# Kernel tuning notes

Hardware: AMD Instinct MI355X
Metric: run time of the kernel (lower is better)

## Reference

```python
import jax, jax.numpy as jnp
import numpy as np

W_SIM, W_REC, W_FREQ, W_IMP, W_TYPE = 0.45, 0.2, 0.15, 0.1, 0.1
TYPE_WEIGHT = 0.9
DECAY_HALF_LIFE = 200.0
TEMPERATURE = 0.07
LN_EPS = 1e-5


def _l2norm(v, axis=-1):
    # matches torch F.normalize (eps=1e-12 clamp on the norm)
    n = jnp.linalg.norm(v, axis=axis, keepdims=True)
    return v / jnp.maximum(n, 1e-12)


def setup_inputs() -> dict:
    key = jax.random.key(0)
    ks = jax.random.split(key, 8)
    B, D, S = 16384, 2048, 64
    s = 1.0 / np.sqrt(D)
    x = jax.random.normal(ks[0], (B, D), jnp.float32)
    prototypes = _l2norm(jax.random.normal(ks[1], (S, D), jnp.float32))
    proto_conf = jax.random.uniform(ks[2], (S,), jnp.float32)
    proto_age = jax.random.uniform(ks[3], (S,), jnp.float32)
    proto_evidence = jnp.ones((S,), jnp.float32)
    W_in = jax.random.normal(ks[4], (D, D), jnp.float32) * s
    b_in = jnp.zeros((D,), jnp.float32)
    Wr1 = jax.random.normal(ks[5], (D // 2, D), jnp.float32) * s
    br1 = jnp.zeros((D // 2,), jnp.float32)
    Wr2 = jax.random.normal(ks[6], (4, D // 2), jnp.float32) * (1.0 / np.sqrt(D // 2))
    br2 = jnp.zeros((4,), jnp.float32)
    W_out = jax.random.normal(ks[7], (D, 2 * D), jnp.float32) * (1.0 / np.sqrt(2 * D))
    b_out = jnp.zeros((D,), jnp.float32)
    ln_w = jnp.ones((D,), jnp.float32)
    ln_b = jnp.zeros((D,), jnp.float32)
    return {"x": x, "prototypes": prototypes, "proto_conf": proto_conf,
            "proto_age": proto_age, "proto_evidence": proto_evidence,
            "W_in": W_in, "b_in": b_in, "Wr1": Wr1, "br1": br1,
            "Wr2": Wr2, "br2": br2, "W_out": W_out, "b_out": b_out,
            "ln_w": ln_w, "ln_b": ln_b}


def reference(x, prototypes, proto_conf, proto_age, proto_evidence,
              W_in, b_in, Wr1, br1, Wr2, br2, W_out, b_out, ln_w, ln_b):
    S = prototypes.shape[0]
    protos_per_type = S // 4

    # in_proj + normalize
    h = x @ W_in.T + b_in                                  # [B, D]
    h_norm = _l2norm(h)

    # type router: Linear -> GELU(exact) -> Linear -> softmax
    r = jax.nn.gelu(x @ Wr1.T + br1, approximate=False)    # [B, D/2]
    type_weights = jax.nn.softmax(r @ Wr2.T + br2, axis=-1)  # [B, 4]

    # prototype similarity
    p_norm = _l2norm(prototypes)
    raw_sim = h_norm @ p_norm.T                            # [B, S]

    type_assign = jnp.arange(S) // protos_per_type         # [S] in {0..3}
    type_mask = type_weights[:, type_assign]               # [B, S]
    weighted_sim = raw_sim * type_mask * proto_conf[None, :]

    # multi-factor salience (fused elementwise)
    recency = jnp.exp(-proto_age / DECAY_HALF_LIFE)[None, :]
    freq_norm = (jnp.log(proto_evidence + 1.0) /
                 (jnp.log(proto_evidence.max() + 2.0) + 1e-8))[None, :]
    sal = (W_SIM * weighted_sim + W_REC * recency + W_FREQ * freq_norm
           + W_IMP * proto_conf[None, :] + W_TYPE * TYPE_WEIGHT)
    sal = jnp.clip(sal, 0.0, 1.0)

    # attention over prototype bank
    attn = jax.nn.softmax(sal / TEMPERATURE, axis=-1)       # [B, S]
    retrieved = attn @ prototypes                           # [B, D]

    combined = jnp.concatenate([x, retrieved], axis=-1)     # [B, 2D]
    out = jax.nn.gelu(combined @ W_out.T + b_out, approximate=False)
    # dropout is identity in eval mode

    # residual + LayerNorm (biased variance, eps=1e-5)
    y = out + x
    mu = jnp.mean(y, axis=-1, keepdims=True)
    var = jnp.mean((y - mu) ** 2, axis=-1, keepdims=True)
    return ln_w * (y - mu) / jnp.sqrt(var + LN_EPS) + ln_b
```

## Files before the change

### kernel.cpp

```cpp
#include <hip/hip_runtime.h>
#include <hip/hip_bf16.h>
#include <cstdint>

#define DEV __device__ __forceinline__

typedef __bf16 bf16x8 __attribute__((ext_vector_type(8)));
typedef float f32x4 __attribute__((ext_vector_type(4)));
typedef unsigned short ushort_t;
typedef ushort_t ushort8 __attribute__((ext_vector_type(8)));

DEV ushort_t f2bf(float f) {
  union { float f; uint32_t u; } x; x.f = f;
  uint32_t r = (x.u + 0x7fffu + ((x.u >> 16) & 1u)) >> 16;
  return (ushort_t)r;
}
DEV float bf2f(ushort_t b) {
  union { uint32_t u; float f; } x; x.u = ((uint32_t)b) << 16;
  return x.f;
}
DEV float gelu_exact(float v) {
  return 0.5f * v * (1.0f + erff(v * 0.70710678118654752f));
}
DEV void gload_lds16(const void* g, void* l) {
  __builtin_amdgcn_global_load_lds(
      (const __attribute__((address_space(1))) void*)g,
      (__attribute__((address_space(3))) void*)l, 16, 0, 0);
}


__global__ __launch_bounds__(64) void prep_scal(
    const float* __restrict__ conf, const float* __restrict__ age,
    const float* __restrict__ ev, float* __restrict__ base, float* __restrict__ cs) {
  int l = threadIdx.x;
  float e = ev[l];
  float m = e;
  #pragma unroll
  for (int d = 1; d < 64; d <<= 1) m = fmaxf(m, __shfl_xor(m, d));
  float freq = logf(e + 1.f) / (logf(m + 2.f) + 1e-8f);
  base[l] = 0.2f * expf(-age[l] * (1.f / 200.f)) + 0.15f * freq + 0.1f * conf[l] + 0.09f;
  cs[l] = 0.45f * conf[l];
}

__global__ __launch_bounds__(256) void prep_pnorm(
    const float* __restrict__ protos, const float* __restrict__ b_in,
    float* __restrict__ p_norm, float* __restrict__ dvec) {
  const int s = blockIdx.x, t = threadIdx.x;
  const float* p = protos + (size_t)s * 2048;
  float vals[8];
  float ss = 0.f, sb = 0.f;
  #pragma unroll
  for (int ii = 0; ii < 2; ++ii) {
    float4 v = *(const float4*)(p + t * 8 + ii * 4);
    float4 bi = *(const float4*)(b_in + t * 8 + ii * 4);
    vals[ii * 4 + 0] = v.x; vals[ii * 4 + 1] = v.y; vals[ii * 4 + 2] = v.z; vals[ii * 4 + 3] = v.w;
    ss += v.x * v.x + v.y * v.y + v.z * v.z + v.w * v.w;
    sb += v.x * bi.x + v.y * bi.y + v.z * bi.z + v.w * bi.w;
  }
  #pragma unroll
  for (int d = 1; d < 64; d <<= 1) { ss += __shfl_xor(ss, d); sb += __shfl_xor(sb, d); }
  __shared__ float red[8];
  if ((t & 63) == 0) { red[t >> 6] = ss; red[4 + (t >> 6)] = sb; }
  __syncthreads();
  ss = red[0] + red[1] + red[2] + red[3];
  sb = red[4] + red[5] + red[6] + red[7];
  float inv = 1.f / fmaxf(sqrtf(ss), 1e-12f);
  #pragma unroll
  for (int k = 0; k < 8; ++k) p_norm[(size_t)s * 2048 + t * 8 + k] = vals[k] * inv;
  if (t == 0) dvec[s] = sb * inv;
}


__global__ __launch_bounds__(256) void conv_x(const float* __restrict__ x, ushort_t* __restrict__ xa) {
  size_t e = ((size_t)blockIdx.x * 256 + threadIdx.x) * 8;
  int row = (int)(e >> 11), col = (int)(e & 2047);
  float4 f0 = *(const float4*)(x + e);
  float4 f1 = *(const float4*)(x + e + 4);
  ushort8 o;
  o[0] = f2bf(f0.x); o[1] = f2bf(f0.y); o[2] = f2bf(f0.z); o[3] = f2bf(f0.w);
  o[4] = f2bf(f1.x); o[5] = f2bf(f1.y); o[6] = f2bf(f1.z); o[7] = f2bf(f1.w);
  *(ushort8*)(xa + (size_t)row * 2112 + col) = o;
}

__global__ __launch_bounds__(256) void conv_wbig(const float* __restrict__ W_in,
                                                 const float* __restrict__ Wr1,
                                                 ushort_t* __restrict__ wbig) {
  size_t e = ((size_t)blockIdx.x * 256 + threadIdx.x) * 8;
  int row = (int)(e >> 11), col = (int)(e & 2047);
  if (row >= 3072 && row < 3136) return;
  ushort8 o;
  if (row < 3072) {
    const float* src = (row < 2048) ? (W_in + (size_t)row * 2048 + col)
                                    : (Wr1 + (size_t)(row - 2048) * 2048 + col);
    float4 f0 = *(const float4*)(src);
    float4 f1 = *(const float4*)(src + 4);
    o[0] = f2bf(f0.x); o[1] = f2bf(f0.y); o[2] = f2bf(f0.z); o[3] = f2bf(f0.w);
    o[4] = f2bf(f1.x); o[5] = f2bf(f1.y); o[6] = f2bf(f1.z); o[7] = f2bf(f1.w);
  } else {
    o = ushort8{0, 0, 0, 0, 0, 0, 0, 0};
  }
  *(ushort8*)(wbig + (size_t)row * 2048 + col) = o;
}

__global__ __launch_bounds__(256) void conv_ww(const float* __restrict__ W_out,
                                               ushort_t* __restrict__ wwm) {
  size_t e = ((size_t)blockIdx.x * 256 + threadIdx.x) * 8;
  int n = (int)(e >> 11), c = (int)(e & 2047);
  float4 f0 = *(const float4*)(W_out + (size_t)n * 4096 + c);
  float4 f1 = *(const float4*)(W_out + (size_t)n * 4096 + c + 4);
  ushort8 o;
  o[0] = f2bf(f0.x); o[1] = f2bf(f0.y); o[2] = f2bf(f0.z); o[3] = f2bf(f0.w);
  o[4] = f2bf(f1.x); o[5] = f2bf(f1.y); o[6] = f2bf(f1.z); o[7] = f2bf(f1.w);
  *(ushort8*)(wwm + (size_t)n * 2112 + c) = o;
}

__global__ __launch_bounds__(256) void small_p2(const float* __restrict__ p_norm,
                                                const float* __restrict__ W_in,
                                                ushort_t* __restrict__ wbig) {
  __shared__ float pn[8][128];
  const int t = threadIdx.x;
  const int k = blockIdx.x * 128 + (t & 127);
  const int sh = t >> 7;
  const int s0 = blockIdx.y * 8;
  float acc[4] = {0.f, 0.f, 0.f, 0.f};
  for (int j0 = 0; j0 < 2048; j0 += 128) {
    __syncthreads();
    {
      int sl = t >> 5;
      int j4 = (t & 31) * 4;
      *(float4*)&pn[sl][j4] = *(const float4*)&p_norm[(size_t)(s0 + sl) * 2048 + j0 + j4];
    }
    __syncthreads();
    #pragma unroll 8
    for (int jj = 0; jj < 128; ++jj) {
      float wv = W_in[(size_t)(j0 + jj) * 2048 + k];
      #pragma unroll
      for (int i = 0; i < 4; ++i) acc[i] += pn[sh * 4 + i][jj] * wv;
    }
  }
  #pragma unroll
  for (int i = 0; i < 4; ++i)
    wbig[(size_t)(3072 + s0 + sh * 4 + i) * 2048 + k] = f2bf(acc[i]);
}

__global__ __launch_bounds__(256) void small_R(const float* __restrict__ protos,
                                               const float* __restrict__ W_out,
                                               ushort_t* __restrict__ wwm) {
  __shared__ float pch[64][68];
  __shared__ float wch[16][68];
  const int t = threadIdx.x;
  const int n_loc = t >> 4;
  const int sb = t & 15;
  const int n0 = blockIdx.x * 16;
  float acc[4] = {0.f, 0.f, 0.f, 0.f};
  for (int k0 = 0; k0 < 2048; k0 += 64) {
    __syncthreads();
    #pragma unroll
    for (int ii = 0; ii < 4; ++ii) {
      int lin4 = t * 4 + ii;
      int s = lin4 >> 4;
      int k4 = (lin4 & 15) * 4;
      *(float4*)&pch[s][k4] = *(const float4*)&protos[(size_t)s * 2048 + k0 + k4];
    }
    {
      int n_l = t >> 4;
      int k4 = (t & 15) * 4;
      *(float4*)&wch[n_l][k4] = *(const float4*)&W_out[(size_t)(n0 + n_l) * 4096 + 2048 + k0 + k4];
    }
    __syncthreads();
    #pragma unroll 8
    for (int kk = 0; kk < 64; ++kk) {
      float wv = wch[n_loc][kk];
      #pragma unroll
      for (int i = 0; i < 4; ++i) acc[i] += pch[sb + 16 * i][kk] * wv;
    }
  }
  #pragma unroll
  for (int i = 0; i < 4; ++i)
    wwm[(size_t)(n0 + n_loc) * 2112 + 2048 + sb + 16 * i] = f2bf(acc[i]);
}

__global__ __launch_bounds__(256) void gemm_head(
    const ushort_t* __restrict__ A, const ushort_t* __restrict__ Bw,
    const float* __restrict__ bias0, const float* __restrict__ bias1,
    float* __restrict__ rn2part, ushort_t* __restrict__ out1, float* __restrict__ out2) {
  __shared__ ushort_t As[128 * 32];
  __shared__ ushort_t Bs[128 * 32];
  const int tid = threadIdx.x;
  const int w = tid >> 6, l = tid & 63;
  const int bm = blockIdx.x * 128;
  const int bn = blockIdx.y * 128;
  const int srow = tid >> 2;
  const int scol = (tid & 3) * 8;
  const int wm = (w >> 1) * 64, wn = (w & 1) * 64;
  const int lr = l & 15, lk = (l >> 4) * 8;

  f32x4 acc[4][4];
  #pragma unroll
  for (int i = 0; i < 4; ++i)
    #pragma unroll
    for (int j = 0; j < 4; ++j) acc[i][j] = f32x4{0.f, 0.f, 0.f, 0.f};

  for (int k0 = 0; k0 < 2048; k0 += 32) {
    __syncthreads();
    #pragma unroll
    for (int r = 0; r < 2; ++r) {
      int row = srow + r * 64;
      gload_lds16(A + (size_t)(bm + row) * 2112 + k0 + scol,
                  (char*)As + (size_t)(r * 256 + tid) * 16);
    }
    #pragma unroll
    for (int r = 0; r < 2; ++r) {
      int row = srow + r * 64;
      gload_lds16(Bw + (size_t)(bn + row) * 2048 + k0 + scol,
                  (char*)Bs + (size_t)(r * 256 + tid) * 16);
    }
    __syncthreads();
    bf16x8 af[4], bf_[4];
    #pragma unroll
    for (int i = 0; i < 4; ++i) af[i] = *(const bf16x8*)&As[(wm + i * 16 + lr) * 32 + lk];
    #pragma unroll
    for (int j = 0; j < 4; ++j) bf_[j] = *(const bf16x8*)&Bs[(wn + j * 16 + lr) * 32 + lk];
    #pragma unroll
    for (int i = 0; i < 4; ++i)
      #pragma unroll
      for (int j = 0; j < 4; ++j)
        acc[i][j] = __builtin_amdgcn_mfma_f32_16x16x32_bf16(af[i], bf_[j], acc[i][j], 0, 0, 0);
  }

  const int lg = l >> 4;
  #pragma unroll
  for (int i = 0; i < 4; ++i) {
    #pragma unroll
    for (int q = 0; q < 4; ++q) {
      const int grow = bm + wm + i * 16 + lg * 4 + q;
      float ss = 0.f;
      #pragma unroll
      for (int j = 0; j < 4; ++j) {
        const int gcol = bn + wn + j * 16 + lr;
        float v = acc[i][j][q];
        if (gcol < 2048) {
          v += bias0[gcol];
          ss += v * v;
        } else if (gcol < 3072) {
          v += bias1[gcol - 2048];
          out1[(size_t)grow * 1024 + (gcol - 2048)] = f2bf(gelu_exact(v));
        } else if (gcol < 3136) {
          out2[(size_t)grow * 64 + (gcol - 3072)] = v;
        }
      }
      if (bn < 2048) {
        ss += __shfl_xor(ss, 1);
        ss += __shfl_xor(ss, 2);
        ss += __shfl_xor(ss, 4);
        ss += __shfl_xor(ss, 8);
        if (lr == 0) rn2part[(size_t)grow * 16 + blockIdx.y] = ss;
      }
    }
  }
}

__global__ __launch_bounds__(256) void gemm_out(
    const ushort_t* __restrict__ A, const ushort_t* __restrict__ Bw,
    const float* __restrict__ bias0, float* __restrict__ out0) {
  __shared__ ushort_t As[128 * 32];
  __shared__ ushort_t Bs[128 * 32];
  const int tid = threadIdx.x;
  const int w = tid >> 6, l = tid & 63;
  const int bm = blockIdx.x * 128;
  const int bn = blockIdx.y * 128;
  const int srow = tid >> 2;
  const int scol = (tid & 3) * 8;
  const int wm = (w >> 1) * 64, wn = (w & 1) * 64;
  const int lr = l & 15, lk = (l >> 4) * 8;

  f32x4 acc[4][4];
  #pragma unroll
  for (int i = 0; i < 4; ++i)
    #pragma unroll
    for (int j = 0; j < 4; ++j) acc[i][j] = f32x4{0.f, 0.f, 0.f, 0.f};

  for (int k0 = 0; k0 < 2112; k0 += 32) {
    __syncthreads();
    #pragma unroll
    for (int r = 0; r < 2; ++r) {
      int row = srow + r * 64;
      gload_lds16(A + (size_t)(bm + row) * 2112 + k0 + scol,
                  (char*)As + (size_t)(r * 256 + tid) * 16);
    }
    #pragma unroll
    for (int r = 0; r < 2; ++r) {
      int row = srow + r * 64;
      gload_lds16(Bw + (size_t)(bn + row) * 2112 + k0 + scol,
                  (char*)Bs + (size_t)(r * 256 + tid) * 16);
    }
    __syncthreads();
    bf16x8 af[4], bf_[4];
    #pragma unroll
    for (int i = 0; i < 4; ++i) af[i] = *(const bf16x8*)&As[(wm + i * 16 + lr) * 32 + lk];
    #pragma unroll
    for (int j = 0; j < 4; ++j) bf_[j] = *(const bf16x8*)&Bs[(wn + j * 16 + lr) * 32 + lk];
    #pragma unroll
    for (int i = 0; i < 4; ++i)
      #pragma unroll
      for (int j = 0; j < 4; ++j)
        acc[i][j] = __builtin_amdgcn_mfma_f32_16x16x32_bf16(af[i], bf_[j], acc[i][j], 0, 0, 0);
  }

  const int lg = l >> 4;
  #pragma unroll
  for (int i = 0; i < 4; ++i)
    #pragma unroll
    for (int j = 0; j < 4; ++j)
      #pragma unroll
      for (int q = 0; q < 4; ++q) {
        const int grow = bm + wm + i * 16 + lg * 4 + q;
        const int gcol = bn + wn + j * 16 + lr;
        float v = acc[i][j][q] + bias0[gcol];
        float g = gelu_exact(v);
        out0[(size_t)grow * 2048 + gcol] = g + bf2f(A[(size_t)grow * 2112 + gcol]);
      }
}

__global__ __launch_bounds__(256) void attn_k(
    const ushort_t* __restrict__ r_bf, const float* __restrict__ Wr2,
    const float* __restrict__ br2, const float* __restrict__ rn2p,
    const float* __restrict__ rproj, const float* __restrict__ dvec,
    const float* __restrict__ base, const float* __restrict__ cs,
    ushort_t* __restrict__ xa) {
  const int b = blockIdx.x * 4 + (threadIdx.x >> 6);
  const int l = threadIdx.x & 63;
  const ushort_t* rrow = r_bf + (size_t)b * 1024;
  float t0 = 0.f, t1 = 0.f, t2 = 0.f, t3 = 0.f;
  #pragma unroll
  for (int m = 0; m < 16; ++m) {
    int k = l + m * 64;
    float rv = bf2f(rrow[k]);
    t0 += rv * Wr2[k];
    t1 += rv * Wr2[1024 + k];
    t2 += rv * Wr2[2048 + k];
    t3 += rv * Wr2[3072 + k];
  }
  #pragma unroll
  for (int d = 1; d < 64; d <<= 1) {
    t0 += __shfl_xor(t0, d); t1 += __shfl_xor(t1, d);
    t2 += __shfl_xor(t2, d); t3 += __shfl_xor(t3, d);
  }
  t0 += br2[0]; t1 += br2[1]; t2 += br2[2]; t3 += br2[3];
  float mx = fmaxf(fmaxf(t0, t1), fmaxf(t2, t3));
  float e0 = expf(t0 - mx), e1 = expf(t1 - mx), e2 = expf(t2 - mx), e3 = expf(t3 - mx);
  float sinv = 1.f / (e0 + e1 + e2 + e3);
  float tw0 = e0 * sinv, tw1 = e1 * sinv, tw2 = e2 * sinv, tw3 = e3 * sinv;
  const int ty = l >> 4;
  float twv = (ty == 0) ? tw0 : ((ty == 1) ? tw1 : ((ty == 2) ? tw2 : tw3));

  float rsum = 0.f;
  #pragma unroll
  for (int t = 0; t < 16; ++t) rsum += rn2p[(size_t)b * 16 + t];
  float inv = 1.f / fmaxf(sqrtf(rsum), 1e-12f);
  float rp = rproj[(size_t)b * 64 + l] + dvec[l];
  float sal = cs[l] * twv * (rp * inv) + base[l];
  sal = fminf(fmaxf(sal, 0.f), 1.f);
  float logit = sal * (1.f / 0.07f);
  float lm = logit;
  #pragma unroll
  for (int d = 1; d < 64; d <<= 1) lm = fmaxf(lm, __shfl_xor(lm, d));
  float ex = expf(logit - lm);
  float es = ex;
  #pragma unroll
  for (int d = 1; d < 64; d <<= 1) es += __shfl_xor(es, d);
  float attn = ex / es;
  xa[(size_t)b * 2112 + 2048 + l] = f2bf(attn);
}

__global__ __launch_bounds__(256) void ln_k(float* __restrict__ y,
                                            const float* __restrict__ lw,
                                            const float* __restrict__ lb) {
  const int b = blockIdx.x, t = threadIdx.x;
  float* row = y + (size_t)b * 2048;
  float4 v0 = *(const float4*)(row + t * 8);
  float4 v1 = *(const float4*)(row + t * 8 + 4);
  float s = v0.x + v0.y + v0.z + v0.w + v1.x + v1.y + v1.z + v1.w;
  float s2 = v0.x * v0.x + v0.y * v0.y + v0.z * v0.z + v0.w * v0.w +
             v1.x * v1.x + v1.y * v1.y + v1.z * v1.z + v1.w * v1.w;
  #pragma unroll
  for (int d = 1; d < 64; d <<= 1) { s += __shfl_xor(s, d); s2 += __shfl_xor(s2, d); }
  __shared__ float red[8];
  if ((t & 63) == 0) { red[t >> 6] = s; red[4 + (t >> 6)] = s2; }
  __syncthreads();
  float ts = red[0] + red[1] + red[2] + red[3];
  float ts2 = red[4] + red[5] + red[6] + red[7];
  const float mu = ts * (1.f / 2048.f);
  const float inv = 1.f / sqrtf(ts2 * (1.f / 2048.f) - mu * mu + 1e-5f);
  float4 w0 = *(const float4*)(lw + t * 8), w1 = *(const float4*)(lw + t * 8 + 4);
  float4 b0 = *(const float4*)(lb + t * 8), b1 = *(const float4*)(lb + t * 8 + 4);
  float4 o0, o1;
  o0.x = (v0.x - mu) * inv * w0.x + b0.x;
  o0.y = (v0.y - mu) * inv * w0.y + b0.y;
  o0.z = (v0.z - mu) * inv * w0.z + b0.z;
  o0.w = (v0.w - mu) * inv * w0.w + b0.w;
  o1.x = (v1.x - mu) * inv * w1.x + b1.x;
  o1.y = (v1.y - mu) * inv * w1.y + b1.y;
  o1.z = (v1.z - mu) * inv * w1.z + b1.z;
  o1.w = (v1.w - mu) * inv * w1.w + b1.w;
  *(float4*)(row + t * 8) = o0;
  *(float4*)(row + t * 8 + 4) = o1;
}

extern "C" void kernel_launch(void* const* d_in, const int* in_sizes, int n_in,
                              void* d_out, int out_size, void* d_ws, size_t ws_size,
                              hipStream_t stream) {
  const float* x      = (const float*)d_in[0];
  const float* protos = (const float*)d_in[1];
  const float* conf   = (const float*)d_in[2];
  const float* age    = (const float*)d_in[3];
  const float* ev     = (const float*)d_in[4];
  const float* W_in   = (const float*)d_in[5];
  const float* b_in   = (const float*)d_in[6];
  const float* Wr1    = (const float*)d_in[7];
  const float* br1    = (const float*)d_in[8];
  const float* Wr2    = (const float*)d_in[9];
  const float* br2    = (const float*)d_in[10];
  const float* W_out  = (const float*)d_in[11];
  const float* b_out  = (const float*)d_in[12];
  const float* ln_w   = (const float*)d_in[13];
  const float* ln_b   = (const float*)d_in[14];
  float* out = (float*)d_out;

  char* ws = (char*)d_ws;
  size_t off = 0;
  auto take = [&](size_t bytes) {
    char* p = ws + off;
    off = (off + bytes + 255) & ~(size_t)255;
    return p;
  };
  ushort_t* xa     = (ushort_t*)take((size_t)16384 * 2112 * 2);
  ushort_t* wbig   = (ushort_t*)take((size_t)3200 * 2048 * 2);
  ushort_t* wwm    = (ushort_t*)take((size_t)2048 * 2112 * 2);
  ushort_t* rbf    = (ushort_t*)take((size_t)16384 * 1024 * 2);
  float*    rproj  = (float*)take((size_t)16384 * 64 * 4);
  float*    rn2p   = (float*)take((size_t)16384 * 16 * 4);
  float*    pnorm  = (float*)take((size_t)64 * 2048 * 4);
  float*    base   = (float*)take(256);
  float*    cs     = (float*)take(256);
  float*    dvec   = (float*)take(256);
  (void)in_sizes; (void)n_in; (void)out_size; (void)ws_size;

  prep_scal<<<1, 64, 0, stream>>>(conf, age, ev, base, cs);
  prep_pnorm<<<64, 256, 0, stream>>>(protos, b_in, pnorm, dvec);
  conv_x<<<16384, 256, 0, stream>>>(x, xa);
  conv_wbig<<<3200, 256, 0, stream>>>(W_in, Wr1, wbig);
  conv_ww<<<2048, 256, 0, stream>>>(W_out, wwm);
  small_p2<<<dim3(16, 8), 256, 0, stream>>>(pnorm, W_in, wbig);
  small_R<<<128, 256, 0, stream>>>(protos, W_out, wwm);
  gemm_head<<<dim3(128, 25), 256, 0, stream>>>(xa, wbig, b_in, br1, rn2p, rbf, rproj);
  attn_k<<<4096, 256, 0, stream>>>(rbf, Wr2, br2, rn2p, rproj, dvec, base, cs, xa);
  gemm_out<<<dim3(128, 16), 256, 0, stream>>>(xa, wwm, b_out, out);
  ln_k<<<16384, 256, 0, stream>>>(out, ln_w, ln_b);
}
```

Baseline: 848.1 us.

## Double-buffer LDS tiles in head and output GEMM main loops

```diff
diff --git a/kernel.cpp b/kernel.cpp
--- a/kernel.cpp
+++ b/kernel.cpp
@@ -183,8 +183,8 @@
     const ushort_t* __restrict__ A, const ushort_t* __restrict__ Bw,
     const float* __restrict__ bias0, const float* __restrict__ bias1,
     float* __restrict__ rn2part, ushort_t* __restrict__ out1, float* __restrict__ out2) {
-  __shared__ ushort_t As[128 * 32];
-  __shared__ ushort_t Bs[128 * 32];
+  __shared__ ushort_t As0[128 * 32], As1[128 * 32];
+  __shared__ ushort_t Bs0[128 * 32], Bs1[128 * 32];
   const int tid = threadIdx.x;
   const int w = tid >> 6, l = tid & 63;
   const int bm = blockIdx.x * 128;
@@ -200,31 +200,38 @@
     #pragma unroll
     for (int j = 0; j < 4; ++j) acc[i][j] = f32x4{0.f, 0.f, 0.f, 0.f};
 
-  for (int k0 = 0; k0 < 2048; k0 += 32) {
-    __syncthreads();
+  auto stage = [&](ushort_t* Ad, ushort_t* Bd, int k0) {
     #pragma unroll
     for (int r = 0; r < 2; ++r) {
       int row = srow + r * 64;
       gload_lds16(A + (size_t)(bm + row) * 2112 + k0 + scol,
-                  (char*)As + (size_t)(r * 256 + tid) * 16);
-    }
-    #pragma unroll
-    for (int r = 0; r < 2; ++r) {
-      int row = srow + r * 64;
+                  (char*)Ad + (size_t)(r * 256 + tid) * 16);
       gload_lds16(Bw + (size_t)(bn + row) * 2048 + k0 + scol,
-                  (char*)Bs + (size_t)(r * 256 + tid) * 16);
-    }
-    __syncthreads();
+                  (char*)Bd + (size_t)(r * 256 + tid) * 16);
+    }
+  };
+  auto compute = [&](const ushort_t* Asrc, const ushort_t* Bsrc) {
     bf16x8 af[4], bf_[4];
     #pragma unroll
-    for (int i = 0; i < 4; ++i) af[i] = *(const bf16x8*)&As[(wm + i * 16 + lr) * 32 + lk];
-    #pragma unroll
-    for (int j = 0; j < 4; ++j) bf_[j] = *(const bf16x8*)&Bs[(wn + j * 16 + lr) * 32 + lk];
+    for (int i = 0; i < 4; ++i) af[i] = *(const bf16x8*)&Asrc[(wm + i * 16 + lr) * 32 + lk];
+    #pragma unroll
+    for (int j = 0; j < 4; ++j) bf_[j] = *(const bf16x8*)&Bsrc[(wn + j * 16 + lr) * 32 + lk];
     #pragma unroll
     for (int i = 0; i < 4; ++i)
       #pragma unroll
       for (int j = 0; j < 4; ++j)
         acc[i][j] = __builtin_amdgcn_mfma_f32_16x16x32_bf16(af[i], bf_[j], acc[i][j], 0, 0, 0);
+  };
+
+  stage(As0, Bs0, 0);
+  __syncthreads();
+  for (int k0 = 0; k0 < 2048; k0 += 64) {
+    if (k0 + 32 < 2048) stage(As1, Bs1, k0 + 32);
+    compute(As0, Bs0);
+    __syncthreads();
+    if (k0 + 64 < 2048) stage(As0, Bs0, k0 + 64);
+    compute(As1, Bs1);
+    __syncthreads();
   }
 
   const int lg = l >> 4;
@@ -262,8 +269,8 @@
 __global__ __launch_bounds__(256) void gemm_out(
     const ushort_t* __restrict__ A, const ushort_t* __restrict__ Bw,
     const float* __restrict__ bias0, float* __restrict__ out0) {
-  __shared__ ushort_t As[128 * 32];
-  __shared__ ushort_t Bs[128 * 32];
+  __shared__ ushort_t As0[128 * 32], As1[128 * 32];
+  __shared__ ushort_t Bs0[128 * 32], Bs1[128 * 32];
   const int tid = threadIdx.x;
   const int w = tid >> 6, l = tid & 63;
   const int bm = blockIdx.x * 128;
@@ -279,31 +286,38 @@
     #pragma unroll
     for (int j = 0; j < 4; ++j) acc[i][j] = f32x4{0.f, 0.f, 0.f, 0.f};
 
-  for (int k0 = 0; k0 < 2112; k0 += 32) {
-    __syncthreads();
+  auto stage = [&](ushort_t* Ad, ushort_t* Bd, int k0) {
     #pragma unroll
     for (int r = 0; r < 2; ++r) {
       int row = srow + r * 64;
       gload_lds16(A + (size_t)(bm + row) * 2112 + k0 + scol,
-                  (char*)As + (size_t)(r * 256 + tid) * 16);
-    }
-    #pragma unroll
-    for (int r = 0; r < 2; ++r) {
-      int row = srow + r * 64;
+                  (char*)Ad + (size_t)(r * 256 + tid) * 16);
       gload_lds16(Bw + (size_t)(bn + row) * 2112 + k0 + scol,
-                  (char*)Bs + (size_t)(r * 256 + tid) * 16);
-    }
-    __syncthreads();
+                  (char*)Bd + (size_t)(r * 256 + tid) * 16);
+    }
+  };
+  auto compute = [&](const ushort_t* Asrc, const ushort_t* Bsrc) {
     bf16x8 af[4], bf_[4];
     #pragma unroll
-    for (int i = 0; i < 4; ++i) af[i] = *(const bf16x8*)&As[(wm + i * 16 + lr) * 32 + lk];
-    #pragma unroll
-    for (int j = 0; j < 4; ++j) bf_[j] = *(const bf16x8*)&Bs[(wn + j * 16 + lr) * 32 + lk];
+    for (int i = 0; i < 4; ++i) af[i] = *(const bf16x8*)&Asrc[(wm + i * 16 + lr) * 32 + lk];
+    #pragma unroll
+    for (int j = 0; j < 4; ++j) bf_[j] = *(const bf16x8*)&Bsrc[(wn + j * 16 + lr) * 32 + lk];
     #pragma unroll
     for (int i = 0; i < 4; ++i)
       #pragma unroll
       for (int j = 0; j < 4; ++j)
         acc[i][j] = __builtin_amdgcn_mfma_f32_16x16x32_bf16(af[i], bf_[j], acc[i][j], 0, 0, 0);
+  };
+
+  stage(As0, Bs0, 0);
+  __syncthreads();
+  for (int k0 = 0; k0 < 2112; k0 += 64) {
+    if (k0 + 32 < 2112) stage(As1, Bs1, k0 + 32);
+    compute(As0, Bs0);
+    __syncthreads();
+    if (k0 + 64 < 2112) stage(As0, Bs0, k0 + 64);
+    compute(As1, Bs1);
+    __syncthreads();
   }
 
   const int lg = l >> 4;
```

After: 923.2 us. +8.9%, slower.
